# Kernel optimization log

Hardware: AMD Instinct MI355X
Metric: run time of the kernel (lower is better)

Reference implementation:

```python
import jax, jax.numpy as jnp
import numpy as np

B, HG, WG = 2, 64, 64
N = HG * WG
C_IN, C_HID, HEADS, C_OUT = 512, 256, 4, 512
NEG_SLOPE = 0.2   # PyG GATv2Conv default negative_slope
LN_EPS = 1e-5


def _grid_edges(h, w):
    """8-neighborhood grid graph, edge_index[0]=source, edge_index[1]=target."""
    nodes = np.arange(h * w).reshape(h, w)
    srcs, dsts = [], []
    for dh in (-1, 0, 1):
        for dw in (-1, 0, 1):
            if dh == 0 and dw == 0:
                continue
            r0, r1 = max(0, -dh), h - max(0, dh)
            c0, c1 = max(0, -dw), w - max(0, dw)
            srcs.append(nodes[r0:r1, c0:c1].ravel())
            dsts.append(nodes[r0 + dh:r1 + dh, c0 + dw:c1 + dw].ravel())
    return np.stack([np.concatenate(srcs), np.concatenate(dsts)]).astype(np.int64)


def setup_inputs() -> dict:
    key = jax.random.key(0)
    ks = iter(jax.random.split(key, 32))

    def p(shape, scale=0.02):
        return jax.random.normal(next(ks), shape, dtype=jnp.float32) * scale

    return {
        "rgb_features": jax.random.normal(next(ks), (B, N, C_IN), dtype=jnp.float32),
        "x_features": jax.random.normal(next(ks), (B, N, C_IN), dtype=jnp.float32),
        "edge_index": jnp.asarray(_grid_edges(HG, WG)),
        # modality_fusion: Linear(2*C_IN, C_HID) + LayerNorm
        "fusion_w": p((C_HID, 2 * C_IN)), "fusion_b": jnp.zeros((C_HID,), jnp.float32),
        "fusion_g": jnp.ones((C_HID,), jnp.float32), "fusion_beta": jnp.zeros((C_HID,), jnp.float32),
        # GATSegmentation.in_proj + norm
        "inproj_w": p((C_HID, C_HID)), "inproj_b": jnp.zeros((C_HID,), jnp.float32),
        "norm_g": jnp.ones((C_HID,), jnp.float32), "norm_b": jnp.zeros((C_HID,), jnp.float32),
        # GATv2Conv layer 0: C_HID -> C_HID, heads=4, concat=True
        "l0_wl": p((HEADS * C_HID, C_HID)), "l0_bl": jnp.zeros((HEADS * C_HID,), jnp.float32),
        "l0_wr": p((HEADS * C_HID, C_HID)), "l0_br": jnp.zeros((HEADS * C_HID,), jnp.float32),
        "l0_att": p((HEADS, C_HID)), "l0_bias": jnp.zeros((HEADS * C_HID,), jnp.float32),
        # GATv2Conv layer 1 (final): 4*C_HID -> C_HID, heads=1, concat=False
        "l1_wl": p((C_HID, HEADS * C_HID)), "l1_bl": jnp.zeros((C_HID,), jnp.float32),
        "l1_wr": p((C_HID, HEADS * C_HID)), "l1_br": jnp.zeros((C_HID,), jnp.float32),
        "l1_att": p((1, C_HID)), "l1_bias": jnp.zeros((C_HID,), jnp.float32),
        # final_proj: 1x1 conv C_HID -> C_OUT
        "fp_w": p((C_OUT, C_HID)), "fp_b": jnp.zeros((C_OUT,), jnp.float32),
    }


def _ln(x, g, b):
    mu = x.mean(-1, keepdims=True)
    v = ((x - mu) ** 2).mean(-1, keepdims=True)
    return (x - mu) * jax.lax.rsqrt(v + LN_EPS) * g + b


def _gatv2(x, src, dst, wl, bl, wr, br, att, bias, concat):
    """PyG GATv2Conv (share_weights=False): gather, leaky_relu logit, segment softmax over
    target neighborhoods, scatter-add aggregation."""
    n = x.shape[0]
    heads, c = att.shape
    xl = (x @ wl.T + bl).reshape(n, heads, c)   # source-side transform (x_j)
    xr = (x @ wr.T + br).reshape(n, heads, c)   # target-side transform (x_i)
    e = jax.nn.leaky_relu(xl[src] + xr[dst], NEG_SLOPE)        # [E, H, C]
    logit = jnp.einsum('ehc,hc->eh', e, att)                   # [E, H]
    m = jax.ops.segment_max(logit, dst, num_segments=n)
    p = jnp.exp(logit - m[dst])
    z = jax.ops.segment_sum(p, dst, num_segments=n)
    alpha = p / z[dst]                                          # softmax per target node
    out = jax.ops.segment_sum(xl[src] * alpha[..., None], dst, num_segments=n)  # [N, H, C]
    out = out.reshape(n, heads * c) if concat else out.mean(axis=1)
    return out + bias


def reference(rgb_features, x_features, edge_index, fusion_w, fusion_b, fusion_g, fusion_beta,
              inproj_w, inproj_b, norm_g, norm_b,
              l0_wl, l0_bl, l0_wr, l0_br, l0_att, l0_bias,
              l1_wl, l1_bl, l1_wr, l1_br, l1_att, l1_bias,
              fp_w, fp_b):
    b, n, _ = rgb_features.shape
    loops = jnp.arange(n, dtype=edge_index.dtype)  # PyG add_self_loops=True
    src = jnp.concatenate([edge_index[0], loops])
    dst = jnp.concatenate([edge_index[1], loops])

    def single(rgb, xm):  # one graph in the batch (original loops over B in Python)
        comb = jnp.concatenate([rgb, xm], axis=-1)                     # [N, 2*C_IN]
        f = jax.nn.relu(_ln(comb @ fusion_w.T + fusion_b, fusion_g, fusion_beta))
        h = jax.nn.relu(_ln(f @ inproj_w.T + inproj_b, norm_g, norm_b))
        h = jax.nn.relu(_gatv2(h, src, dst, l0_wl, l0_bl, l0_wr, l0_br, l0_att, l0_bias, True))
        h = jax.nn.relu(_gatv2(h, src, dst, l1_wl, l1_bl, l1_wr, l1_br, l1_att, l1_bias, False))
        return h                                                        # [N, C_HID]

    nodes = jax.vmap(single)(rgb_features, x_features)                  # [B, N, C_HID]
    img = nodes.reshape(b, HG, WG, C_HID)
    return jnp.einsum('bhwc,oc->bohw', img, fp_w) + fp_b[None, :, None, None]
```

## Files before the change

kernel.cpp:

```cpp
#include <hip/hip_runtime.h>


#define NNODE 4096
#define LN_EPS 1e-5f
#define LOG2E 1.4426950408889634f

typedef _Float16 half8 __attribute__((ext_vector_type(8)));
typedef _Float16 half4 __attribute__((ext_vector_type(4)));
typedef _Float16 h2 __attribute__((ext_vector_type(2)));
typedef float f32x4 __attribute__((ext_vector_type(4)));

__device__ __forceinline__ float wave_reduce_sum(float v) {
    #pragma unroll
    for (int off = 32; off > 0; off >>= 1) v += __shfl_xor(v, off, 64);
    return v;
}

__device__ __forceinline__ void gload_lds16(const void* g, void* l) {
    __builtin_amdgcn_global_load_lds(
        (const __attribute__((address_space(1))) void*)g,
        (__attribute__((address_space(3))) void*)l, 16, 0, 0);
}

template<int N> __device__ __forceinline__ void waitcnt_vm() {
    if constexpr (N <= 0)      asm volatile("s_waitcnt vmcnt(0)" ::: "memory");
    else if constexpr (N == 2) asm volatile("s_waitcnt vmcnt(2)" ::: "memory");
    else if constexpr (N == 3) asm volatile("s_waitcnt vmcnt(3)" ::: "memory");
    else if constexpr (N == 4) asm volatile("s_waitcnt vmcnt(4)" ::: "memory");
    else                       asm volatile("s_waitcnt vmcnt(8)" ::: "memory");
}
__device__ __forceinline__ void barrier_raw() {
    asm volatile("s_barrier" ::: "memory");
}

__device__ __forceinline__ int xcd_swz(int lin, int total) {
    return (lin & 7) * (total >> 3) + (lin >> 3);
}

template<int IT, int JT, int OUTMODE>
__global__ __launch_bounds__(256) void gemm3_k(
    const _Float16* __restrict__ A, const _Float16* __restrict__ W,
    const float* __restrict__ bias_lo, const float* __restrict__ bias_hi,
    int nsplit, void* __restrict__ Cout, int K, int N)
{
    constexpr int BM = 32 * IT, BN = 32 * JT;
    constexpr int CA = (BM * 4) / 256;
    constexpr int CB = (BN * 4) / 256;
    constexpr int L = CA + CB;
    __shared__ _Float16 ldsA[3][BM * 32];
    __shared__ _Float16 ldsB[3][BN * 32];

    const int tid = threadIdx.x;
    const int lin = blockIdx.y * gridDim.x + blockIdx.x;
    const int swz = xcd_swz(lin, gridDim.x * gridDim.y);
    const int m0 = (swz / gridDim.x) * BM, n0 = (swz % gridDim.x) * BN;
    const int lane = tid & 63, w = tid >> 6;
    const int fr = lane & 15, kq = lane >> 4;
    const int sq = (kq ^ (fr & 3)) * 8;
    const int wm = (w & 1) * (16 * IT), wn = (w >> 1) * (16 * JT);

    const _Float16* aP[CA]; int aC[CA];
    #pragma unroll
    for (int i = 0; i < CA; ++i) {
        const int c = i * 256 + tid, r = c >> 2, q = (c & 3) ^ (r & 3);
        aP[i] = A + (size_t)(m0 + r) * K + q * 8;
        aC[i] = c * 8;
    }
    const _Float16* bP[CB]; int bC[CB];
    #pragma unroll
    for (int i = 0; i < CB; ++i) {
        const int c = i * 256 + tid, r = c >> 2, q = (c & 3) ^ (r & 3);
        bP[i] = W + (size_t)(n0 + r) * K + q * 8;
        bC[i] = c * 8;
    }

    f32x4 acc[IT][JT] = {};
    const int NT = K >> 5;

    #pragma unroll
    for (int i = 0; i < CA; ++i) gload_lds16(aP[i], &ldsA[0][aC[i]]);
    #pragma unroll
    for (int i = 0; i < CB; ++i) gload_lds16(bP[i], &ldsB[0][bC[i]]);
    #pragma unroll
    for (int i = 0; i < CA; ++i) gload_lds16(aP[i] + 32, &ldsA[1][aC[i]]);
    #pragma unroll
    for (int i = 0; i < CB; ++i) gload_lds16(bP[i] + 32, &ldsB[1][bC[i]]);

    int bi = 0;
    for (int t = 0; t < NT; ++t) {
        if (t + 1 < NT) waitcnt_vm<L>(); else waitcnt_vm<0>();
        barrier_raw();
        if (t + 2 < NT) {
            int nb = bi + 2; if (nb >= 3) nb -= 3;
            const int k2 = (t + 2) << 5;
            #pragma unroll
            for (int i = 0; i < CA; ++i) gload_lds16(aP[i] + k2, &ldsA[nb][aC[i]]);
            #pragma unroll
            for (int i = 0; i < CB; ++i) gload_lds16(bP[i] + k2, &ldsB[nb][bC[i]]);
        }
        half8 af[IT], bf[JT];
        #pragma unroll
        for (int i = 0; i < IT; ++i)
            af[i] = *(const half8*)&ldsA[bi][(wm + i * 16 + fr) * 32 + sq];
        #pragma unroll
        for (int j = 0; j < JT; ++j)
            bf[j] = *(const half8*)&ldsB[bi][(wn + j * 16 + fr) * 32 + sq];
        #pragma unroll
        for (int i = 0; i < IT; ++i)
            #pragma unroll
            for (int j = 0; j < JT; ++j) {
                if (OUTMODE == 1)
                    acc[i][j] = __builtin_amdgcn_mfma_f32_16x16x32_f16(
                        bf[j], af[i], acc[i][j], 0, 0, 0);
                else
                    acc[i][j] = __builtin_amdgcn_mfma_f32_16x16x32_f16(
                        af[i], bf[j], acc[i][j], 0, 0, 0);
            }
        ++bi; if (bi == 3) bi = 0;
    }

    if (OUTMODE == 1) {
        #pragma unroll
        for (int i = 0; i < IT; ++i) {
            const int m = m0 + wm + i * 16 + fr;
            #pragma unroll
            for (int j = 0; j < JT; ++j) {
                const int nb4 = n0 + wn + j * 16 + kq * 4;
                const float* bp = (nb4 < nsplit) ? bias_lo + nb4
                                                 : bias_hi + (nb4 - nsplit);
                const float4 bv = *(const float4*)bp;
                half4 ov = {(_Float16)(acc[i][j][0] + bv.x),
                            (_Float16)(acc[i][j][1] + bv.y),
                            (_Float16)(acc[i][j][2] + bv.z),
                            (_Float16)(acc[i][j][3] + bv.w)};
                *(half4*)((_Float16*)Cout + (size_t)m * N + nb4) = ov;
            }
        }
    } else {
        #pragma unroll
        for (int j = 0; j < JT; ++j) {
            const int col = n0 + wn + j * 16 + fr;
            const float bc = (col < nsplit) ? bias_lo[col] : bias_hi[col - nsplit];
            #pragma unroll
            for (int i = 0; i < IT; ++i) {
                const int mrun = m0 + wm + i * 16 + kq * 4;
                const int b = mrun >> 12, node = mrun & 4095;
                float4 ov = {acc[i][j][0] + bc, acc[i][j][1] + bc,
                             acc[i][j][2] + bc, acc[i][j][3] + bc};
                *(float4*)((float*)Cout + ((size_t)(b * N + col)) * 4096 + node) = ov;
            }
        }
    }
}

__global__ __launch_bounds__(512) void fusion3_k(
    const _Float16* __restrict__ Af,
    const _Float16* __restrict__ W1, const float* __restrict__ b1,
    const float* __restrict__ g1, const float* __restrict__ be1,
    const _Float16* __restrict__ W2, const float* __restrict__ b2,
    const float* __restrict__ g2, const float* __restrict__ be2,
    _Float16* __restrict__ out)
{
    __shared__ _Float16 lA[3][16 * 32];
    __shared__ _Float16 lB[3][256 * 32];
    __shared__ float lC[16 * 260];
    __shared__ _Float16 lH[8 * 512];

    const int tid = threadIdx.x;
    const int m0 = blockIdx.x * 16;
    const int lane = tid & 63, w = tid >> 6;
    const int fr = lane & 15, kq = lane >> 4;
    const int sq = (kq ^ (fr & 3)) * 8;
    const int wc = w * 32;
    const bool stager = (tid < 64);

    const _Float16* bP[2]; int bC[2];
    #pragma unroll
    for (int i = 0; i < 2; ++i) {
        const int c = i * 512 + tid, r = c >> 2, q = (c & 3) ^ (r & 3);
        bP[i] = W1 + (size_t)r * 1024 + q * 8;
        bC[i] = c * 8;
    }
    const int arow = tid >> 2, aq = (tid & 3) ^ (arow & 3);
    const _Float16* aP = Af + (size_t)(m0 + arow) * 1024 + aq * 8;
    const int aC = tid * 8;

    f32x4 acc[2] = {};

    if (stager) gload_lds16(aP, &lA[0][aC]);
    #pragma unroll
    for (int i = 0; i < 2; ++i) gload_lds16(bP[i], &lB[0][bC[i]]);
    if (stager) gload_lds16(aP + 32, &lA[1][aC]);
    #pragma unroll
    for (int i = 0; i < 2; ++i) gload_lds16(bP[i] + 32, &lB[1][bC[i]]);

    int bi = 0;
    for (int t = 0; t < 32; ++t) {
        if (t + 1 < 32) { if (stager) waitcnt_vm<3>(); else waitcnt_vm<2>(); }
        else            waitcnt_vm<0>();
        barrier_raw();
        if (t + 2 < 32) {
            int nb = bi + 2; if (nb >= 3) nb -= 3;
            const int k2 = (t + 2) << 5;
            if (stager) gload_lds16(aP + k2, &lA[nb][aC]);
            #pragma unroll
            for (int i = 0; i < 2; ++i) gload_lds16(bP[i] + k2, &lB[nb][bC[i]]);
        }
        const half8 af = *(const half8*)&lA[bi][fr * 32 + sq];
        half8 bf[2];
        #pragma unroll
        for (int j = 0; j < 2; ++j)
            bf[j] = *(const half8*)&lB[bi][(wc + j * 16 + fr) * 32 + sq];
        #pragma unroll
        for (int j = 0; j < 2; ++j)
            acc[j] = __builtin_amdgcn_mfma_f32_16x16x32_f16(af, bf[j], acc[j], 0, 0, 0);
        ++bi; if (bi == 3) bi = 0;
    }

    #pragma unroll
    for (int j = 0; j < 2; ++j) {
        const int col = wc + j * 16 + fr;
        const float bc = b1[col];
        #pragma unroll
        for (int r4 = 0; r4 < 4; ++r4)
            lC[(kq * 4 + r4) * 260 + col] = acc[j][r4] + bc;
    }
    __syncthreads();

    {
        const float4 gv = *(const float4*)(g1 + lane * 4);
        const float4 bv = *(const float4*)(be1 + lane * 4);
        const int t2i = lane >> 3, gq = (lane >> 1) & 3, qo = (lane & 1) * 4;
        #pragma unroll
        for (int rr = 0; rr < 2; ++rr) {
            const int row = w * 2 + rr;
            const float4 v = *(const float4*)&lC[row * 260 + lane * 4];
            float s  = v.x + v.y + v.z + v.w;
            float s2 = v.x * v.x + v.y * v.y + v.z * v.z + v.w * v.w;
            s = wave_reduce_sum(s);
            s2 = wave_reduce_sum(s2);
            const float mu  = s * (1.0f / 256.0f);
            const float var = s2 * (1.0f / 256.0f) - mu * mu;
            const float rs  = rsqrtf(var + LN_EPS);
            half4 o;
            o[0] = (_Float16)fmaxf((v.x - mu) * rs * gv.x + bv.x, 0.f);
            o[1] = (_Float16)fmaxf((v.y - mu) * rs * gv.y + bv.y, 0.f);
            o[2] = (_Float16)fmaxf((v.z - mu) * rs * gv.z + bv.z, 0.f);
            o[3] = (_Float16)fmaxf((v.w - mu) * rs * gv.w + bv.w, 0.f);
            const int qslot = gq ^ (row & 3);
            *(half4*)&lH[t2i * 512 + (row * 4 + qslot) * 8 + qo] = o;
        }
    }
    __syncthreads();

    const _Float16* b2P[2]; int b2C[2];
    #pragma unroll
    for (int i = 0; i < 2; ++i) {
        const int c = i * 512 + tid, r = c >> 2, q = (c & 3) ^ (r & 3);
        b2P[i] = W2 + (size_t)r * 256 + q * 8;
        b2C[i] = c * 8;
    }
    f32x4 acc2[2] = {};
    #pragma unroll
    for (int i = 0; i < 2; ++i) gload_lds16(b2P[i], &lB[0][b2C[i]]);
    #pragma unroll
    for (int i = 0; i < 2; ++i) gload_lds16(b2P[i] + 32, &lB[1][b2C[i]]);

    int bi2 = 0;
    for (int t2 = 0; t2 < 8; ++t2) {
        if (t2 + 1 < 8) waitcnt_vm<2>(); else waitcnt_vm<0>();
        barrier_raw();
        if (t2 + 2 < 8) {
            int nb = bi2 + 2; if (nb >= 3) nb -= 3;
            const int k2 = (t2 + 2) << 5;
            #pragma unroll
            for (int i = 0; i < 2; ++i) gload_lds16(b2P[i] + k2, &lB[nb][b2C[i]]);
        }
        const half8 af = *(const half8*)
            &lH[t2 * 512 + (fr * 4 + (kq ^ (fr & 3))) * 8];
        half8 bf[2];
        #pragma unroll
        for (int j = 0; j < 2; ++j)
            bf[j] = *(const half8*)&lB[bi2][(wc + j * 16 + fr) * 32 + sq];
        #pragma unroll
        for (int j = 0; j < 2; ++j)
            acc2[j] = __builtin_amdgcn_mfma_f32_16x16x32_f16(af, bf[j], acc2[j], 0, 0, 0);
        ++bi2; if (bi2 == 3) bi2 = 0;
    }

    __syncthreads();
    #pragma unroll
    for (int j = 0; j < 2; ++j) {
        const int col = wc + j * 16 + fr;
        const float bc = b2[col];
        #pragma unroll
        for (int r4 = 0; r4 < 4; ++r4)
            lC[(kq * 4 + r4) * 260 + col] = acc2[j][r4] + bc;
    }
    __syncthreads();

    {
        const float4 gv = *(const float4*)(g2 + lane * 4);
        const float4 bv = *(const float4*)(be2 + lane * 4);
        #pragma unroll
        for (int rr = 0; rr < 2; ++rr) {
            const int row = w * 2 + rr;
            const float4 v = *(const float4*)&lC[row * 260 + lane * 4];
            float s  = v.x + v.y + v.z + v.w;
            float s2 = v.x * v.x + v.y * v.y + v.z * v.z + v.w * v.w;
            s = wave_reduce_sum(s);
            s2 = wave_reduce_sum(s2);
            const float mu  = s * (1.0f / 256.0f);
            const float var = s2 * (1.0f / 256.0f) - mu * mu;
            const float rs  = rsqrtf(var + LN_EPS);
            half4 o;
            o[0] = (_Float16)fmaxf((v.x - mu) * rs * gv.x + bv.x, 0.f);
            o[1] = (_Float16)fmaxf((v.y - mu) * rs * gv.y + bv.y, 0.f);
            o[2] = (_Float16)fmaxf((v.z - mu) * rs * gv.z + bv.z, 0.f);
            o[3] = (_Float16)fmaxf((v.w - mu) * rs * gv.w + bv.w, 0.f);
            *(half4*)(out + (size_t)(m0 + row) * 256 + lane * 4) = o;
        }
    }
}

template<int HEADS, int LD, int XROFF, int OC>
__global__ __launch_bounds__(256) void gat4_k(
    const _Float16* __restrict__ xlr, const _Float16* __restrict__ att16,
    const float* __restrict__ bias, _Float16* __restrict__ out)
{
    const int tid = threadIdx.x, wv = tid >> 6, lane = tid & 63;
    const int g = lane >> 4, li = lane & 15;
    const int blk = xcd_swz(blockIdx.x, gridDim.x);
    const int wid = blk * 4 + wv;
    const int gi = (HEADS == 4) ? wid : wid * 4 + g;
    const int h  = (HEADS == 4) ? g : 0;
    const int node = gi & (NNODE - 1);
    const int base = gi - node;
    const int nr = node >> 6, nc = node & 63;
    const int co = h * 256 + li * 16;

    int sidx[9]; float msk[9];
    {
        const int drs[8] = {-1,-1,-1, 0, 0, 1, 1, 1};
        const int dcs[8] = {-1, 0, 1,-1, 1,-1, 0, 1};
        #pragma unroll
        for (int j = 0; j < 8; ++j) {
            const int rj = nr + drs[j], cj = nc + dcs[j];
            const bool v = ((unsigned)rj < 64u) & ((unsigned)cj < 64u);
            sidx[j] = v ? (rj * 64 + cj) : node;
            msk[j] = v ? 0.f : -1e30f;
        }
        sidx[8] = node; msk[8] = 0.f;
    }

    const _Float16* xp = xlr + (size_t)base * LD + co;

    half8 x0[9], x1[9];
    #pragma unroll
    for (int j = 0; j < 9; ++j) {
        x0[j] = *(const half8*)(xp + (size_t)sidx[j] * LD);
        x1[j] = *(const half8*)(xp + (size_t)sidx[j] * LD + 8);
    }
    const half8 xr0 = *(const half8*)(xlr + (size_t)gi * LD + XROFF + co);
    const half8 xr1 = *(const half8*)(xlr + (size_t)gi * LD + XROFF + co + 8);
    const half8 at0 = *(const half8*)(att16 + h * 256 + li * 16);
    const half8 at1 = *(const half8*)(att16 + h * 256 + li * 16 + 8);
    const h2 hz = {(_Float16)0.f, (_Float16)0.f};
    const h2 c02 = {(_Float16)0.2f, (_Float16)0.2f};

    float lg[9];
    #pragma unroll
    for (int j = 0; j < 9; ++j) {
        h2 p = hz;
        #pragma unroll
        for (int k = 0; k < 4; ++k) {
            h2 e = ((const h2*)&x0[j])[k] + ((const h2*)&xr0)[k];
            h2 tt = __builtin_elementwise_fma(
                __builtin_elementwise_min(e, hz), c02,
                __builtin_elementwise_max(e, hz));
            p = __builtin_elementwise_fma(tt, ((const h2*)&at0)[k], p);
        }
        #pragma unroll
        for (int k = 0; k < 4; ++k) {
            h2 e = ((const h2*)&x1[j])[k] + ((const h2*)&xr1)[k];
            h2 tt = __builtin_elementwise_fma(
                __builtin_elementwise_min(e, hz), c02,
                __builtin_elementwise_max(e, hz));
            p = __builtin_elementwise_fma(tt, ((const h2*)&at1)[k], p);
        }
        float pl = (float)p[0] + (float)p[1];
        pl += __shfl_xor(pl, 1, 64);
        pl += __shfl_xor(pl, 2, 64);
        pl += __shfl_xor(pl, 4, 64);
        pl += __shfl_xor(pl, 8, 64);
        lg[j] = pl + msk[j];
    }

    float m = lg[0];
    #pragma unroll
    for (int j = 1; j < 9; ++j) m = fmaxf(m, lg[j]);
    float pj[9], z = 0.f;
    #pragma unroll
    for (int j = 0; j < 9; ++j) { pj[j] = __builtin_amdgcn_exp2f(lg[j] - m); z += pj[j]; }
    const float inv = __builtin_amdgcn_rcpf(z);

    float acc[16];
    #pragma unroll
    for (int k = 0; k < 16; ++k) acc[k] = 0.f;
    #pragma unroll
    for (int j = 0; j < 9; ++j) {
        const float wj = pj[j];
        #pragma unroll
        for (int k = 0; k < 8; ++k) acc[k]     += wj * (float)x0[j][k];
        #pragma unroll
        for (int k = 0; k < 8; ++k) acc[8 + k] += wj * (float)x1[j][k];
    }
    float bv[16];
    #pragma unroll
    for (int q = 0; q < 4; ++q) {
        const float4 b4 = *(const float4*)(bias + h * 256 + li * 16 + q * 4);
        bv[q * 4 + 0] = b4.x; bv[q * 4 + 1] = b4.y;
        bv[q * 4 + 2] = b4.z; bv[q * 4 + 3] = b4.w;
    }
    half8 o0, o1;
    #pragma unroll
    for (int k = 0; k < 8; ++k) o0[k] = (_Float16)fmaxf(acc[k] * inv + bv[k], 0.f);
    #pragma unroll
    for (int k = 0; k < 8; ++k) o1[k] = (_Float16)fmaxf(acc[8 + k] * inv + bv[8 + k], 0.f);
    *(half8*)(out + (size_t)gi * OC + co) = o0;
    *(half8*)(out + (size_t)gi * OC + co + 8) = o1;
}

struct WTab {
    const float* src[9];
    int startblk[10];
    int nelem[9];
    int dstoff[9];
    float scale[9];
};

__global__ __launch_bounds__(256) void prep_k(
    const float* __restrict__ rgb, const float* __restrict__ xm,
    _Float16* __restrict__ Cf16, WTab t, _Float16* __restrict__ dst)
{
    if (blockIdx.x < 4096) {
        const int idx = blockIdx.x * 256 + threadIdx.x;
        const int m = idx >> 7;
        const int k = (idx & 127) * 8;
        const float* s = (k < 512) ? rgb + (size_t)m * 512 + k
                                   : xm  + (size_t)m * 512 + (k - 512);
        const float4 v0 = *(const float4*)s;
        const float4 v1 = *(const float4*)(s + 4);
        half8 o = {(_Float16)v0.x, (_Float16)v0.y, (_Float16)v0.z, (_Float16)v0.w,
                   (_Float16)v1.x, (_Float16)v1.y, (_Float16)v1.z, (_Float16)v1.w};
        *(half8*)(Cf16 + (size_t)m * 1024 + k) = o;
        return;
    }
    const int b = blockIdx.x - 4096;
    int s = 0;
    #pragma unroll
    for (int i = 1; i < 9; ++i) s += (b >= t.startblk[i]);
    const int e0 = (b - t.startblk[s]) * 1024 + threadIdx.x * 4;
    if (e0 >= t.nelem[s]) return;
    const float4 v = *(const float4*)(t.src[s] + e0);
    const float sc = t.scale[s];
    half4 o = {(_Float16)(v.x * sc), (_Float16)(v.y * sc),
               (_Float16)(v.z * sc), (_Float16)(v.w * sc)};
    *(half4*)(dst + t.dstoff[s] + e0) = o;
}

extern "C" void kernel_launch(void* const* d_in, const int* in_sizes, int n_in,
                              void* d_out, int out_size, void* d_ws, size_t ws_size,
                              hipStream_t stream)
{
    const float* rgb       = (const float*)d_in[0];
    const float* xm        = (const float*)d_in[1];
    const float* fusion_w  = (const float*)d_in[3];
    const float* fusion_b  = (const float*)d_in[4];
    const float* fusion_g  = (const float*)d_in[5];
    const float* fusion_be = (const float*)d_in[6];
    const float* inproj_w  = (const float*)d_in[7];
    const float* inproj_b  = (const float*)d_in[8];
    const float* norm_g    = (const float*)d_in[9];
    const float* norm_b    = (const float*)d_in[10];
    const float* l0_wl     = (const float*)d_in[11];
    const float* l0_bl     = (const float*)d_in[12];
    const float* l0_wr     = (const float*)d_in[13];
    const float* l0_br     = (const float*)d_in[14];
    const float* l0_att    = (const float*)d_in[15];
    const float* l0_bias   = (const float*)d_in[16];
    const float* l1_wl     = (const float*)d_in[17];
    const float* l1_bl     = (const float*)d_in[18];
    const float* l1_wr     = (const float*)d_in[19];
    const float* l1_br     = (const float*)d_in[20];
    const float* l1_att    = (const float*)d_in[21];
    const float* l1_bias   = (const float*)d_in[22];
    const float* fp_w      = (const float*)d_in[23];
    const float* fp_b      = (const float*)d_in[24];

    char* ws = (char*)d_ws;
    _Float16* Wf16 = (_Float16*)ws;
    _Float16* H1   = (_Float16*)(ws + 4194304);
    _Float16* XLR0 = (_Float16*)(ws + 8388608);
    _Float16* GO0  = (_Float16*)(ws + 41943040);
    _Float16* XLR1 = (_Float16*)(ws + 58720256);
    _Float16* GO1  = (_Float16*)(ws + 67108864);
    _Float16* Cf16 = (_Float16*)(ws + 71303168);

    _Float16* w_fus  = Wf16 + 0;
    _Float16* w_inp  = Wf16 + 262144;
    _Float16* w_l0   = Wf16 + 327680;
    _Float16* w_l1   = Wf16 + 851968;
    _Float16* w_fp   = Wf16 + 1376256;
    _Float16* att0_h = Wf16 + 1507328;
    _Float16* att1_h = Wf16 + 1508352;

    WTab t;
    const float* srcs[9] = {fusion_w, inproj_w, l0_wl, l0_wr, l1_wl, l1_wr,
                            fp_w, l0_att, l1_att};
    const int nel[9]  = {262144, 65536, 262144, 262144, 262144, 262144,
                         131072, 1024, 256};
    const int doff[9] = {0, 262144, 327680, 589824, 851968, 1114112,
                         1376256, 1507328, 1508352};
    const int sblk[10] = {0, 256, 320, 576, 832, 1088, 1344, 1472, 1473, 1474};
    for (int i = 0; i < 9; ++i) {
        t.src[i] = srcs[i]; t.nelem[i] = nel[i]; t.dstoff[i] = doff[i];
        t.scale[i] = (i >= 7) ? LOG2E : 1.0f;
    }
    for (int i = 0; i < 10; ++i) t.startblk[i] = sblk[i];

    prep_k<<<4096 + 1474, 256, 0, stream>>>(rgb, xm, Cf16, t, Wf16);

    fusion3_k<<<512, 512, 0, stream>>>(
        Cf16, w_fus, fusion_b, fusion_g, fusion_be,
        w_inp, inproj_b, norm_g, norm_b, H1);

    gemm3_k<4, 4, 1><<<dim3(16, 64), 256, 0, stream>>>(
        H1, w_l0, l0_bl, l0_br, 1024, XLR0, 256, 2048);

    gat4_k<4, 2048, 1024, 1024><<<2048, 256, 0, stream>>>(
        XLR0, att0_h, l0_bias, GO0);

    gemm3_k<2, 4, 1><<<dim3(4, 128), 256, 0, stream>>>(
        GO0, w_l1, l1_bl, l1_br, 256, XLR1, 1024, 512);

    gat4_k<1, 512, 256, 256><<<512, 256, 0, stream>>>(
        XLR1, att1_h, l1_bias, GO1);

    gemm3_k<2, 4, 2><<<dim3(4, 128), 256, 0, stream>>>(
        GO1, w_fp, fp_b, fp_b, 512, d_out, 256, 512);
}
```

Measured before the change: 118.4 us.

## Double fusion kernel row tile to 32 rows with 1024-thread blocks

After: 117.1 us. No clear change (-1.1%).

```diff
diff --git a/kernel.cpp b/kernel.cpp
--- a/kernel.cpp
+++ b/kernel.cpp
@@ -24,6 +24,7 @@
 
 template<int N> __device__ __forceinline__ void waitcnt_vm() {
     if constexpr (N <= 0)      asm volatile("s_waitcnt vmcnt(0)" ::: "memory");
+    else if constexpr (N == 1) asm volatile("s_waitcnt vmcnt(1)" ::: "memory");
     else if constexpr (N == 2) asm volatile("s_waitcnt vmcnt(2)" ::: "memory");
     else if constexpr (N == 3) asm volatile("s_waitcnt vmcnt(3)" ::: "memory");
     else if constexpr (N == 4) asm volatile("s_waitcnt vmcnt(4)" ::: "memory");
@@ -153,7 +154,7 @@
     }
 }
 
-__global__ __launch_bounds__(512) void fusion3_k(
+__global__ __launch_bounds__(1024) void fusion4_k(
     const _Float16* __restrict__ Af,
     const _Float16* __restrict__ W1, const float* __restrict__ b1,
     const float* __restrict__ g1, const float* __restrict__ be1,
@@ -161,26 +162,22 @@
     const float* __restrict__ g2, const float* __restrict__ be2,
     _Float16* __restrict__ out)
 {
-    __shared__ _Float16 lA[3][16 * 32];
+    __shared__ _Float16 lA[3][32 * 32];
     __shared__ _Float16 lB[3][256 * 32];
-    __shared__ float lC[16 * 260];
-    __shared__ _Float16 lH[8 * 512];
+    __shared__ float lC[32 * 260];
+    __shared__ _Float16 lH[8 * 1024];
 
     const int tid = threadIdx.x;
-    const int m0 = blockIdx.x * 16;
+    const int m0 = blockIdx.x * 32;
     const int lane = tid & 63, w = tid >> 6;
     const int fr = lane & 15, kq = lane >> 4;
     const int sq = (kq ^ (fr & 3)) * 8;
-    const int wc = w * 32;
-    const bool stager = (tid < 64);
-
-    const _Float16* bP[2]; int bC[2];
-    #pragma unroll
-    for (int i = 0; i < 2; ++i) {
-        const int c = i * 512 + tid, r = c >> 2, q = (c & 3) ^ (r & 3);
-        bP[i] = W1 + (size_t)r * 1024 + q * 8;
-        bC[i] = c * 8;
-    }
+    const int wr = (w & 1) * 16, wc = (w >> 1) * 32;
+    const bool stager = (tid < 128);
+
+    const int bc_ = tid, br_ = bc_ >> 2, bq_ = (bc_ & 3) ^ (br_ & 3);
+    const _Float16* bP = W1 + (size_t)br_ * 1024 + bq_ * 8;
+    const int bC = bc_ * 8;
     const int arow = tid >> 2, aq = (tid & 3) ^ (arow & 3);
     const _Float16* aP = Af + (size_t)(m0 + arow) * 1024 + aq * 8;
     const int aC = tid * 8;
@@ -188,25 +185,22 @@
     f32x4 acc[2] = {};
 
     if (stager) gload_lds16(aP, &lA[0][aC]);
-    #pragma unroll
-    for (int i = 0; i < 2; ++i) gload_lds16(bP[i], &lB[0][bC[i]]);
+    gload_lds16(bP, &lB[0][bC]);
     if (stager) gload_lds16(aP + 32, &lA[1][aC]);
-    #pragma unroll
-    for (int i = 0; i < 2; ++i) gload_lds16(bP[i] + 32, &lB[1][bC[i]]);
+    gload_lds16(bP + 32, &lB[1][bC]);
 
     int bi = 0;
     for (int t = 0; t < 32; ++t) {
-        if (t + 1 < 32) { if (stager) waitcnt_vm<3>(); else waitcnt_vm<2>(); }
+        if (t + 1 < 32) { if (stager) waitcnt_vm<2>(); else waitcnt_vm<1>(); }
         else            waitcnt_vm<0>();
         barrier_raw();
         if (t + 2 < 32) {
             int nb = bi + 2; if (nb >= 3) nb -= 3;
             const int k2 = (t + 2) << 5;
             if (stager) gload_lds16(aP + k2, &lA[nb][aC]);
-            #pragma unroll
-            for (int i = 0; i < 2; ++i) gload_lds16(bP[i] + k2, &lB[nb][bC[i]]);
-        }
-        const half8 af = *(const half8*)&lA[bi][fr * 32 + sq];
+            gload_lds16(bP + k2, &lB[nb][bC]);
+        }
+        const half8 af = *(const half8*)&lA[bi][(wr + fr) * 32 + sq];
         half8 bf[2];
         #pragma unroll
         for (int j = 0; j < 2; ++j)
@@ -223,7 +217,7 @@
         const float bc = b1[col];
         #pragma unroll
         for (int r4 = 0; r4 < 4; ++r4)
-            lC[(kq * 4 + r4) * 260 + col] = acc[j][r4] + bc;
+            lC[(wr + kq * 4 + r4) * 260 + col] = acc[j][r4] + bc;
     }
     __syncthreads();
 
@@ -248,36 +242,27 @@
             o[2] = (_Float16)fmaxf((v.z - mu) * rs * gv.z + bv.z, 0.f);
             o[3] = (_Float16)fmaxf((v.w - mu) * rs * gv.w + bv.w, 0.f);
             const int qslot = gq ^ (row & 3);
-            *(half4*)&lH[t2i * 512 + (row * 4 + qslot) * 8 + qo] = o;
+            *(half4*)&lH[t2i * 1024 + (row * 4 + qslot) * 8 + qo] = o;
         }
     }
     __syncthreads();
 
-    const _Float16* b2P[2]; int b2C[2];
-    #pragma unroll
-    for (int i = 0; i < 2; ++i) {
-        const int c = i * 512 + tid, r = c >> 2, q = (c & 3) ^ (r & 3);
-        b2P[i] = W2 + (size_t)r * 256 + q * 8;
-        b2C[i] = c * 8;
-    }
+    const int b2r = tid >> 2, b2q = (tid & 3) ^ (b2r & 3);
+    const _Float16* b2P = W2 + (size_t)b2r * 256 + b2q * 8;
     f32x4 acc2[2] = {};
-    #pragma unroll
-    for (int i = 0; i < 2; ++i) gload_lds16(b2P[i], &lB[0][b2C[i]]);
-    #pragma unroll
-    for (int i = 0; i < 2; ++i) gload_lds16(b2P[i] + 32, &lB[1][b2C[i]]);
+    gload_lds16(b2P, &lB[0][bC]);
+    gload_lds16(b2P + 32, &lB[1][bC]);
 
     int bi2 = 0;
     for (int t2 = 0; t2 < 8; ++t2) {
-        if (t2 + 1 < 8) waitcnt_vm<2>(); else waitcnt_vm<0>();
+        if (t2 + 1 < 8) waitcnt_vm<1>(); else waitcnt_vm<0>();
         barrier_raw();
         if (t2 + 2 < 8) {
             int nb = bi2 + 2; if (nb >= 3) nb -= 3;
-            const int k2 = (t2 + 2) << 5;
-            #pragma unroll
-            for (int i = 0; i < 2; ++i) gload_lds16(b2P[i] + k2, &lB[nb][b2C[i]]);
+            gload_lds16(b2P + ((t2 + 2) << 5), &lB[nb][bC]);
         }
         const half8 af = *(const half8*)
-            &lH[t2 * 512 + (fr * 4 + (kq ^ (fr & 3))) * 8];
+            &lH[t2 * 1024 + ((wr + fr) * 4 + (kq ^ (fr & 3))) * 8];
         half8 bf[2];
         #pragma unroll
         for (int j = 0; j < 2; ++j)
@@ -295,7 +280,7 @@
         const float bc = b2[col];
         #pragma unroll
         for (int r4 = 0; r4 < 4; ++r4)
-            lC[(kq * 4 + r4) * 260 + col] = acc2[j][r4] + bc;
+            lC[(wr + kq * 4 + r4) * 260 + col] = acc2[j][r4] + bc;
     }
     __syncthreads();
 
@@ -531,7 +516,7 @@
 
     prep_k<<<4096 + 1474, 256, 0, stream>>>(rgb, xm, Cf16, t, Wf16);
 
-    fusion3_k<<<512, 512, 0, stream>>>(
+    fusion4_k<<<256, 1024, 0, stream>>>(
         Cf16, w_fus, fusion_b, fusion_g, fusion_be,
         w_inp, inproj_b, norm_g, norm_b, H1);
 
```
